# Kernel tuning notes

Measured on AMD Instinct MI355X. Metric: run time of the kernel, lower is better.

## Reference

```python
import jax, jax.numpy as jnp
import numpy as np

DIM = 2048
HIDDEN = 2048
HEADS = 4
HD = HIDDEN // HEADS  # head_dim = 512
EPS = 1e-6
BATCH = 4
SEQ = 2048


def setup_inputs() -> dict:
    key = jax.random.key(0)
    k0, k1, k2, k3 = jax.random.split(key, 4)
    s = 0.02  # typical init scale; keeps exp() input gate well-behaved
    x = jax.random.normal(k0, (BATCH, SEQ, DIM), dtype=jnp.float32)
    W_in = (jax.random.normal(k1, (HIDDEN, DIM), dtype=jnp.float32) * s)
    W_gate = (jax.random.normal(k2, (4 * HIDDEN, HIDDEN), dtype=jnp.float32) * s)
    b_gate = jnp.zeros((4 * HIDDEN,), dtype=jnp.float32)
    rms_w = jnp.ones((HD,), dtype=jnp.float32)
    W_out = (jax.random.normal(k3, (DIM, HIDDEN), dtype=jnp.float32) * s)
    return {"x": x, "W_in": W_in, "W_gate": W_gate, "b_gate": b_gate,
            "rms_w": rms_w, "W_out": W_out}


def reference(x, W_in, W_gate, b_gate, rms_w, W_out):
    B, L, _ = x.shape
    # in_proj then gate_proj (the rearrange round-trip in torch is an identity
    # on the flat hidden dim, so gates come straight from x @ W_in.T)
    xp = x @ W_in.T                                    # (B, L, HIDDEN)
    gates = xp @ W_gate.T + b_gate                     # (B, L, 4*HIDDEN)
    # rearrange 'b l (h d) -> b h l d' with h=HEADS, d=4*HD
    gates = gates.reshape(B, L, HEADS, 4 * HD).transpose(0, 2, 1, 3)
    i_g, f_g, o_g, c_t = jnp.split(gates, 4, axis=-1)  # each (B, H, L, HD)
    i_g = jnp.exp(i_g)            # exponential input gate
    f_g = jax.nn.sigmoid(f_g)
    o_g = jax.nn.sigmoid(o_g)
    c_t = jnp.tanh(c_t)

    # time-major for the recurrent scan: (L, B, H, HD)
    tm = lambda a: jnp.moveaxis(a, 2, 0)

    def step(c, g):
        i, f, o, cd = g
        c = f * c + i * cd                                         # cell update
        c_norm = c * jax.lax.rsqrt(jnp.mean(c * c, axis=-1, keepdims=True) + EPS) * rms_w
        h = o * jnp.tanh(c_norm)
        return c, h

    c0 = jnp.zeros((B, HEADS, HD), dtype=x.dtype)
    _, hs = jax.lax.scan(step, c0, (tm(i_g), tm(f_g), tm(o_g), tm(c_t)))
    # (L, B, H, HD) -> (B, L, H*HD)
    h_out = jnp.moveaxis(hs, 0, 1).reshape(B, L, HIDDEN)
    return h_out @ W_out.T                             # (B, L, DIM)
```

## Files before the change

### kernel.cpp

```cpp
#include <hip/hip_runtime.h>
#include <hip/hip_bf16.h>
#include <stdint.h>

#define DIMN    2048
#define HIDDEN  2048
#define NHEADS  4
#define HDIM    512
#define BATCH   4
#define SEQ     2048
#define NTOK    (BATCH*SEQ)
#define G4      (4*HIDDEN)
#define EPSV    1e-6f
#define CHUNK   128
#define NCHUNK  (SEQ/CHUNK)

typedef short short8 __attribute__((ext_vector_type(8)));
typedef float floatx4 __attribute__((ext_vector_type(4)));

union BV8 { uint4 u; __hip_bfloat16 h[8]; unsigned short s[8]; };

__device__ __forceinline__ float fast_sigmoid(float x) {
    return 1.0f / (1.0f + __expf(-x));
}
__device__ __forceinline__ float fast_tanh(float x) {
    return 1.0f - 2.0f / (__expf(2.0f * x) + 1.0f);
}
__device__ __forceinline__ float b2f(unsigned short u) {
    union { unsigned int ui; float f; } v; v.ui = ((unsigned int)u) << 16; return v.f;
}

__device__ __forceinline__ void gld_lds16(const void* gp, void* lp) {
    __builtin_amdgcn_global_load_lds(
        (const __attribute__((address_space(1))) void*)gp,
        (__attribute__((address_space(3))) void*)lp, 16, 0, 0);
}

__global__ __launch_bounds__(256) void cast_f32_bf16(
    const float* __restrict__ in, __hip_bfloat16* __restrict__ out, int n8)
{
    int i = blockIdx.x * 256 + threadIdx.x;
    if (i >= n8) return;
    const float4* p = (const float4*)(in + (size_t)i * 8);
    float4 a = p[0], b = p[1];
    BV8 v;
    v.h[0] = __float2bfloat16(a.x); v.h[1] = __float2bfloat16(a.y);
    v.h[2] = __float2bfloat16(a.z); v.h[3] = __float2bfloat16(a.w);
    v.h[4] = __float2bfloat16(b.x); v.h[5] = __float2bfloat16(b.y);
    v.h[6] = __float2bfloat16(b.z); v.h[7] = __float2bfloat16(b.w);
    *(uint4*)(out + (size_t)i * 8) = v.u;
}

template <int EPILOGUE, int ASRC>
__global__ __launch_bounds__(512, 2) void gemm256(
    const __hip_bfloat16* __restrict__ A,
    const __hip_bfloat16* __restrict__ Bt,
    void* __restrict__ Cout,
    const float* __restrict__ bias,
    int M, int N, int K, int lda)
{
    __shared__ __align__(16) short sA[2][256 * 64];
    __shared__ __align__(16) short sB[2][256 * 64];

    const int tid  = threadIdx.x;
    const int wave = tid >> 6, lane = tid & 63;
    const int wm = wave >> 2, wn = wave & 3;
    const int quad = lane >> 4, lr = lane & 15;
    const int r8  = lane >> 3;
    const int gcs = ((lane & 7) ^ r8) * 8;
    const int rl7 = lr & 7;

    const int gx   = gridDim.x;
    const int nwg  = gx * gridDim.y;
    const int orig = blockIdx.y * gx + blockIdx.x;
    const int wg   = (orig & 7) * (nwg >> 3) + (orig >> 3);
    const int bm = wg / gx, bn = wg % gx;

    const short* Ag = (const short*)A + (size_t)(bm * 256) * lda;
    const short* Bg = (const short*)Bt + (size_t)(bn * 256) * K;

    floatx4 acc[8][4];
#pragma unroll
    for (int i = 0; i < 8; ++i)
#pragma unroll
        for (int j = 0; j < 4; ++j) acc[i][j] = (floatx4)0.0f;

    const int NT = K >> 6;

    auto stageA = [&](int kt, int qm) {
        const int kb = kt << 6;
        size_t acol;
        if (ASRC == 0) acol = (size_t)(kb + gcs);
        else           acol = (size_t)(((kb >> 9) << 11) + (kb & 511) + gcs);
        short* dst = &sA[kt & 1][0];
#pragma unroll
        for (int e = 0; e < 2; ++e) {
            const int base = qm * 128 + e * 64 + wave * 8;
            const int row  = base + r8;
            const int grow = ((row >> 6) & 1) * 128 + qm * 64 + (row & 63);
            gld_lds16(Ag + (size_t)grow * lda + acol, dst + base * 64);
        }
    };
    auto stageB = [&](int kt, int qn) {
        const int kb = kt << 6;
        short* dst = &sB[kt & 1][0];
#pragma unroll
        for (int e = 0; e < 2; ++e) {
            const int base = qn * 128 + e * 64 + wave * 8;
            const int row  = base + r8;
            const int grow = ((row >> 5) & 3) * 64 + qn * 32 + (row & 31);
            gld_lds16(Bg + (size_t)grow * K + kb + gcs, dst + base * 64);
        }
    };

    stageA(0, 0); stageB(0, 0); stageB(0, 1); stageA(0, 1);
    stageA(1, 0); stageB(1, 0); stageB(1, 1);
    asm volatile("s_waitcnt vmcnt(6)" ::: "memory");
    __builtin_amdgcn_s_barrier();

    short8 av[4][2], b0[2][2], b1[2][2];

    for (int t = 0; t < NT; ++t) {
        const short* lA = &sA[t & 1][0];
        const short* lB = &sB[t & 1][0];

#pragma unroll
        for (int kc = 0; kc < 2; ++kc) {
            const int co = (((kc * 4 + quad) ^ rl7) << 3);
#pragma unroll
            for (int m = 0; m < 4; ++m)
                av[m][kc] = *(const short8*)&lA[(wm * 64 + m * 16 + lr) * 64 + co];
#pragma unroll
            for (int j = 0; j < 2; ++j)
                b0[j][kc] = *(const short8*)&lB[(wn * 32 + j * 16 + lr) * 64 + co];
        }
        if (t + 1 < NT) stageA(t + 1, 1);
        __builtin_amdgcn_s_setprio(1);
#pragma unroll
        for (int m = 0; m < 4; ++m)
#pragma unroll
            for (int j = 0; j < 2; ++j)
#pragma unroll
                for (int kc = 0; kc < 2; ++kc)
                    acc[m][j] = __builtin_amdgcn_mfma_f32_16x16x32_bf16(
                        av[m][kc], b0[j][kc], acc[m][j], 0, 0, 0);
        __builtin_amdgcn_s_setprio(0);
        __builtin_amdgcn_s_barrier();

#pragma unroll
        for (int kc = 0; kc < 2; ++kc) {
            const int co = (((kc * 4 + quad) ^ rl7) << 3);
#pragma unroll
            for (int j = 0; j < 2; ++j)
                b1[j][kc] = *(const short8*)&lB[(128 + wn * 32 + j * 16 + lr) * 64 + co];
        }
        if (t + 2 < NT) stageA(t + 2, 0);
        __builtin_amdgcn_s_setprio(1);
#pragma unroll
        for (int m = 0; m < 4; ++m)
#pragma unroll
            for (int j = 0; j < 2; ++j)
#pragma unroll
                for (int kc = 0; kc < 2; ++kc)
                    acc[m][2 + j] = __builtin_amdgcn_mfma_f32_16x16x32_bf16(
                        av[m][kc], b1[j][kc], acc[m][2 + j], 0, 0, 0);
        __builtin_amdgcn_s_setprio(0);
        __builtin_amdgcn_s_barrier();

#pragma unroll
        for (int kc = 0; kc < 2; ++kc) {
            const int co = (((kc * 4 + quad) ^ rl7) << 3);
#pragma unroll
            for (int m = 0; m < 4; ++m)
                av[m][kc] = *(const short8*)&lA[(128 + wm * 64 + m * 16 + lr) * 64 + co];
        }
        if (t + 2 < NT) stageB(t + 2, 0);
        __builtin_amdgcn_s_setprio(1);
#pragma unroll
        for (int m = 0; m < 4; ++m)
#pragma unroll
            for (int j = 0; j < 2; ++j)
#pragma unroll
                for (int kc = 0; kc < 2; ++kc)
                    acc[4 + m][2 + j] = __builtin_amdgcn_mfma_f32_16x16x32_bf16(
                        av[m][kc], b1[j][kc], acc[4 + m][2 + j], 0, 0, 0);
        __builtin_amdgcn_s_setprio(0);
        __builtin_amdgcn_s_barrier();

        if (t + 2 < NT) stageB(t + 2, 1);
        __builtin_amdgcn_s_setprio(1);
#pragma unroll
        for (int m = 0; m < 4; ++m)
#pragma unroll
            for (int j = 0; j < 2; ++j)
#pragma unroll
                for (int kc = 0; kc < 2; ++kc)
                    acc[4 + m][j] = __builtin_amdgcn_mfma_f32_16x16x32_bf16(
                        av[m][kc], b0[j][kc], acc[4 + m][j], 0, 0, 0);
        __builtin_amdgcn_s_setprio(0);
        if (t < NT - 2)       asm volatile("s_waitcnt vmcnt(6)" ::: "memory");
        else if (t == NT - 2) asm volatile("s_waitcnt vmcnt(0)" ::: "memory");
        __builtin_amdgcn_s_barrier();
    }

    const int colbase = bn * 256 + wn * 64;
    const int rowbase = bm * 256 + wm * 128;

    if (EPILOGUE == 0) {
        __hip_bfloat16* O = (__hip_bfloat16*)Cout;
#pragma unroll
        for (int mt = 0; mt < 8; ++mt)
#pragma unroll
            for (int nt = 0; nt < 4; ++nt)
#pragma unroll
                for (int r = 0; r < 4; ++r) {
                    int row = rowbase + mt * 16 + quad * 4 + r;
                    int col = colbase + nt * 16 + lr;
                    O[(size_t)row * N + col] = __float2bfloat16(acc[mt][nt][r]);
                }
    } else if (EPILOGUE == 1) {
        __hip_bfloat16* O = (__hip_bfloat16*)Cout;
#pragma unroll
        for (int nt = 0; nt < 4; ++nt) {
            int col = colbase + nt * 16 + lr;
            int g = (col >> 9) & 3;
            float bv = bias[col];
#pragma unroll
            for (int mt = 0; mt < 8; ++mt)
#pragma unroll
                for (int r = 0; r < 4; ++r) {
                    int row = rowbase + mt * 16 + quad * 4 + r;
                    float v = acc[mt][nt][r] + bv;
                    if (g == 0)       v = __expf(v);
                    else if (g == 3)  v = fast_tanh(v);
                    else              v = fast_sigmoid(v);
                    O[(size_t)row * N + col] = __float2bfloat16(v);
                }
        }
    } else {
        float* O = (float*)Cout;
#pragma unroll
        for (int mt = 0; mt < 8; ++mt)
#pragma unroll
            for (int nt = 0; nt < 4; ++nt)
#pragma unroll
                for (int r = 0; r < 4; ++r) {
                    int row = rowbase + mt * 16 + quad * 4 + r;
                    int col = colbase + nt * 16 + lr;
                    O[(size_t)row * N + col] = acc[mt][nt][r];
                }
    }
}

struct G16 { unsigned short i[16], f[16], c[16]; };

__device__ __forceinline__ void load_g16(const unsigned short* __restrict__ g,
                                         int t0, G16& o)
{
#pragma unroll
    for (int j = 0; j < 16; ++j) {
        const unsigned short* gp = g + (size_t)(t0 + j) * G4;
        o.i[j] = gp[0]; o.f[j] = gp[512]; o.c[j] = gp[1536];
    }
}
__device__ __forceinline__ void comp_sum16(const G16& gg, float& c, float& P)
{
#pragma unroll
    for (int j = 0; j < 16; ++j) {
        float iv = b2f(gg.i[j]);
        float fv = b2f(gg.f[j]);
        float cd = b2f(gg.c[j]);
        c = fmaf(fv, c, iv * cd);
        P *= fv;
    }
}
__device__ __forceinline__ float comp_store16(const G16& gg, float c,
                                              __hip_bfloat16* __restrict__ cb, int t0)
{
#pragma unroll
    for (int j = 0; j < 16; ++j) {
        float iv = b2f(gg.i[j]);
        float fv = b2f(gg.f[j]);
        float cd = b2f(gg.c[j]);
        c = fmaf(fv, c, iv * cd);
        cb[(size_t)(t0 + j) * HIDDEN] = __float2bfloat16(c);
    }
    return c;
}

__global__ __launch_bounds__(256) void scan_pass1(
    const __hip_bfloat16* __restrict__ gates,
    float* __restrict__ cLast, float* __restrict__ PLast)
{
    int blk = blockIdx.x;
    int dh = blk & 1;
    int j  = (blk >> 1) & 15;
    int bh = blk >> 5;
    int b = bh >> 2, h = bh & 3;
    int d = dh * 256 + threadIdx.x;
    int bhd = bh * 512 + d;

    const unsigned short* g = (const unsigned short*)gates
        + (size_t)(b * SEQ + j * CHUNK) * G4 + h * 2048 + d;

    float c = 0.0f, P = 1.0f;
    G16 A, B;
    load_g16(g, 0, A);
    for (int t0 = 0; t0 < CHUNK; t0 += 32) {
        load_g16(g, t0 + 16, B);
        comp_sum16(A, c, P);
        if (t0 + 32 < CHUNK) load_g16(g, t0 + 32, A);
        comp_sum16(B, c, P);
    }
    cLast[j * 8192 + bhd] = c;
    PLast[j * 8192 + bhd] = P;
}

__global__ __launch_bounds__(256) void scan_pass2(
    const __hip_bfloat16* __restrict__ gates,
    const float* __restrict__ cLast, const float* __restrict__ PLast,
    __hip_bfloat16* __restrict__ cbuf)
{
    int blk = blockIdx.x;
    int dh = blk & 1;
    int j  = (blk >> 1) & 15;
    int bh = blk >> 5;
    int b = bh >> 2, h = bh & 3;
    int d = dh * 256 + threadIdx.x;
    int bhd = bh * 512 + d;

    float c = 0.0f;
    for (int k = 0; k < j; ++k)
        c = fmaf(PLast[k * 8192 + bhd], c, cLast[k * 8192 + bhd]);

    const unsigned short* g = (const unsigned short*)gates
        + (size_t)(b * SEQ + j * CHUNK) * G4 + h * 2048 + d;
    __hip_bfloat16* cb = cbuf
        + (size_t)(b * SEQ + j * CHUNK) * HIDDEN + h * 512 + d;

    G16 A, B;
    load_g16(g, 0, A);
    for (int t0 = 0; t0 < CHUNK; t0 += 32) {
        load_g16(g, t0 + 16, B);
        c = comp_store16(A, c, cb, t0);
        if (t0 + 32 < CHUNK) load_g16(g, t0 + 32, A);
        c = comp_store16(B, c, cb, t0 + 16);
    }
}

__global__ __launch_bounds__(64) void norm_kernel(
    const __hip_bfloat16* __restrict__ cbuf, __hip_bfloat16* __restrict__ gates,
    const float* __restrict__ rms_w)
{
    int blk = blockIdx.x;
    int h = blk & 3;
    int t = (blk >> 2) & (SEQ - 1);
    int b = blk >> 13;
    int lane = threadIdx.x;
    size_t tok = (size_t)(b * SEQ + t);

    BV8 cv; cv.u = *(const uint4*)(cbuf + tok * HIDDEN + h * 512 + lane * 8);
    float cf[8]; float s = 0.0f;
#pragma unroll
    for (int j = 0; j < 8; ++j) { cf[j] = b2f(cv.s[j]); s += cf[j] * cf[j]; }
#pragma unroll
    for (int off = 32; off > 0; off >>= 1) s += __shfl_xor(s, off, 64);
    float rs = rsqrtf(s * (1.0f / 512.0f) + EPSV);

    BV8 ov; ov.u = *(const uint4*)(gates + tok * G4 + h * 2048 + 1024 + lane * 8);
    float4 w0 = *(const float4*)&rms_w[lane * 8];
    float4 w1 = *(const float4*)&rms_w[lane * 8 + 4];
    float w[8] = { w0.x, w0.y, w0.z, w0.w, w1.x, w1.y, w1.z, w1.w };

    BV8 hv;
#pragma unroll
    for (int j = 0; j < 8; ++j) {
        float o = b2f(ov.s[j]);
        hv.h[j] = __float2bfloat16(o * fast_tanh(cf[j] * rs * w[j]));
    }
    *(uint4*)(gates + tok * G4 + h * 2048 + lane * 8) = hv.u;
}

extern "C" void kernel_launch(void* const* d_in, const int* in_sizes, int n_in,
                              void* d_out, int out_size, void* d_ws, size_t ws_size,
                              hipStream_t stream)
{
    const float* x      = (const float*)d_in[0];
    const float* W_in   = (const float*)d_in[1];
    const float* W_gate = (const float*)d_in[2];
    const float* b_gate = (const float*)d_in[3];
    const float* rms_w  = (const float*)d_in[4];
    const float* W_out  = (const float*)d_in[5];
    float* out = (float*)d_out;

    char* base = (char*)d_ws;
    __hip_bfloat16* wgb   = (__hip_bfloat16*)base;
    __hip_bfloat16* xpb   = (__hip_bfloat16*)(base + (((size_t)32) << 20));
    __hip_bfloat16* gates = (__hip_bfloat16*)(base + (((size_t)64) << 20));
    __hip_bfloat16* wib  = gates;
    __hip_bfloat16* xb   = (__hip_bfloat16*)(base + (((size_t)72) << 20));
    __hip_bfloat16* wob  = wgb;
    float* cLast = (float*)(base + (((size_t)8) << 20));
    float* PLast = (float*)(base + (((size_t)8) << 20) + (512 << 10));
    __hip_bfloat16* cbuf = xpb;

    cast_f32_bf16<<<(HIDDEN * DIMN) / 8 / 256, 256, 0, stream>>>(W_in, wib, (HIDDEN * DIMN) / 8);
    cast_f32_bf16<<<(NTOK * DIMN) / 8 / 256, 256, 0, stream>>>(x, xb, (NTOK * DIMN) / 8);
    cast_f32_bf16<<<(G4 * HIDDEN) / 8 / 256, 256, 0, stream>>>(W_gate, wgb, (G4 * HIDDEN) / 8);

    {
        dim3 grid(HIDDEN / 256, NTOK / 256);
        gemm256<0, 0><<<grid, 512, 0, stream>>>(xb, wib, xpb, nullptr,
                                                NTOK, HIDDEN, DIMN, DIMN);
    }
    {
        dim3 grid(G4 / 256, NTOK / 256);
        gemm256<1, 0><<<grid, 512, 0, stream>>>(xpb, wgb, gates, b_gate,
                                                NTOK, G4, HIDDEN, HIDDEN);
    }
    cast_f32_bf16<<<(DIMN * HIDDEN) / 8 / 256, 256, 0, stream>>>(W_out, wob, (DIMN * HIDDEN) / 8);

    scan_pass1<<<BATCH * NHEADS * NCHUNK * 2, 256, 0, stream>>>(gates, cLast, PLast);
    scan_pass2<<<BATCH * NHEADS * NCHUNK * 2, 256, 0, stream>>>(gates, cLast, PLast, cbuf);

    norm_kernel<<<BATCH * SEQ * NHEADS, 64, 0, stream>>>(cbuf, gates, rms_w);

    {
        dim3 grid(DIMN / 256, NTOK / 256);
        gemm256<2, 1><<<grid, 512, 0, stream>>>(gates, wob, out, nullptr,
                                                NTOK, DIMN, HIDDEN, G4);
    }
}
```

Before: 632.9 us.

## Fuse scan pass2 with RMS norm via shared-memory cell buffer

Merges the second scan pass and the per-token RMS-norm/output-gate kernel into one kernel. Each block now covers a full head (512 threads) for one 128-step chunk and keeps the cell states in a 128 KB shared array instead of writing them to global memory. The norm then reads them back from LDS. This removes a global round trip of the cell buffer and one launch. In exchange it cuts the pass-2 grid from 512 to 256 blocks, and the large shared allocation limits occupancy to about one block per CU.

```diff
diff --git a/kernel.cpp b/kernel.cpp
--- a/kernel.cpp
+++ b/kernel.cpp
@@ -273,8 +273,9 @@
         P *= fv;
     }
 }
-__device__ __forceinline__ float comp_store16(const G16& gg, float c,
-                                              __hip_bfloat16* __restrict__ cb, int t0)
+__device__ __forceinline__ float comp_lds16(const G16& gg, float c,
+                                            __hip_bfloat16* __restrict__ sc,
+                                            int t0, int d)
 {
 #pragma unroll
     for (int j = 0; j < 16; ++j) {
@@ -282,7 +283,7 @@
         float fv = b2f(gg.f[j]);
         float cd = b2f(gg.c[j]);
         c = fmaf(fv, c, iv * cd);
-        cb[(size_t)(t0 + j) * HIDDEN] = __float2bfloat16(c);
+        sc[(t0 + j) * HDIM + d] = __float2bfloat16(c);
     }
     return c;
 }
@@ -315,69 +316,65 @@
     PLast[j * 8192 + bhd] = P;
 }
 
-__global__ __launch_bounds__(256) void scan_pass2(
-    const __hip_bfloat16* __restrict__ gates,
+__global__ __launch_bounds__(512) void scan_pass2_norm(
+    const __hip_bfloat16* __restrict__ gates_c,
     const float* __restrict__ cLast, const float* __restrict__ PLast,
-    __hip_bfloat16* __restrict__ cbuf)
-{
+    __hip_bfloat16* __restrict__ gates,
+    const float* __restrict__ rms_w)
+{
+    __shared__ __hip_bfloat16 sc[CHUNK * HDIM];
+
     int blk = blockIdx.x;
-    int dh = blk & 1;
-    int j  = (blk >> 1) & 15;
-    int bh = blk >> 5;
+    int j  = blk & 15;
+    int bh = blk >> 4;
     int b = bh >> 2, h = bh & 3;
-    int d = dh * 256 + threadIdx.x;
+    int d = threadIdx.x;
     int bhd = bh * 512 + d;
 
     float c = 0.0f;
     for (int k = 0; k < j; ++k)
         c = fmaf(PLast[k * 8192 + bhd], c, cLast[k * 8192 + bhd]);
 
-    const unsigned short* g = (const unsigned short*)gates
+    const unsigned short* g = (const unsigned short*)gates_c
         + (size_t)(b * SEQ + j * CHUNK) * G4 + h * 2048 + d;
-    __hip_bfloat16* cb = cbuf
-        + (size_t)(b * SEQ + j * CHUNK) * HIDDEN + h * 512 + d;
 
     G16 A, B;
     load_g16(g, 0, A);
     for (int t0 = 0; t0 < CHUNK; t0 += 32) {
         load_g16(g, t0 + 16, B);
-        c = comp_store16(A, c, cb, t0);
+        c = comp_lds16(A, c, sc, t0, d);
         if (t0 + 32 < CHUNK) load_g16(g, t0 + 32, A);
-        c = comp_store16(B, c, cb, t0 + 16);
-    }
-}
-
-__global__ __launch_bounds__(64) void norm_kernel(
-    const __hip_bfloat16* __restrict__ cbuf, __hip_bfloat16* __restrict__ gates,
-    const float* __restrict__ rms_w)
-{
-    int blk = blockIdx.x;
-    int h = blk & 3;
-    int t = (blk >> 2) & (SEQ - 1);
-    int b = blk >> 13;
-    int lane = threadIdx.x;
-    size_t tok = (size_t)(b * SEQ + t);
-
-    BV8 cv; cv.u = *(const uint4*)(cbuf + tok * HIDDEN + h * 512 + lane * 8);
-    float cf[8]; float s = 0.0f;
-#pragma unroll
-    for (int j = 0; j < 8; ++j) { cf[j] = b2f(cv.s[j]); s += cf[j] * cf[j]; }
-#pragma unroll
-    for (int off = 32; off > 0; off >>= 1) s += __shfl_xor(s, off, 64);
-    float rs = rsqrtf(s * (1.0f / 512.0f) + EPSV);
-
-    BV8 ov; ov.u = *(const uint4*)(gates + tok * G4 + h * 2048 + 1024 + lane * 8);
+        c = comp_lds16(B, c, sc, t0 + 16, d);
+    }
+    __syncthreads();
+
+    const int wave = threadIdx.x >> 6, lane = threadIdx.x & 63;
+
     float4 w0 = *(const float4*)&rms_w[lane * 8];
     float4 w1 = *(const float4*)&rms_w[lane * 8 + 4];
     float w[8] = { w0.x, w0.y, w0.z, w0.w, w1.x, w1.y, w1.z, w1.w };
 
-    BV8 hv;
-#pragma unroll
-    for (int j = 0; j < 8; ++j) {
-        float o = b2f(ov.s[j]);
-        hv.h[j] = __float2bfloat16(o * fast_tanh(cf[j] * rs * w[j]));
-    }
-    *(uint4*)(gates + tok * G4 + h * 2048 + lane * 8) = hv.u;
+    for (int it = 0; it < 16; ++it) {
+        int t = wave * 16 + it;
+        size_t tok = (size_t)(b * SEQ + j * CHUNK + t);
+
+        BV8 cv; cv.u = *(const uint4*)&sc[t * HDIM + lane * 8];
+        float cf[8]; float s = 0.0f;
+#pragma unroll
+        for (int q = 0; q < 8; ++q) { cf[q] = b2f(cv.s[q]); s += cf[q] * cf[q]; }
+#pragma unroll
+        for (int off = 32; off > 0; off >>= 1) s += __shfl_xor(s, off, 64);
+        float rs = rsqrtf(s * (1.0f / 512.0f) + EPSV);
+
+        BV8 ov; ov.u = *(const uint4*)(gates + tok * G4 + h * 2048 + 1024 + lane * 8);
+        BV8 hv;
+#pragma unroll
+        for (int q = 0; q < 8; ++q) {
+            float o = b2f(ov.s[q]);
+            hv.h[q] = __float2bfloat16(o * fast_tanh(cf[q] * rs * w[q]));
+        }
+        *(uint4*)(gates + tok * G4 + h * 2048 + lane * 8) = hv.u;
+    }
 }
 
 extern "C" void kernel_launch(void* const* d_in, const int* in_sizes, int n_in,
@@ -401,7 +398,6 @@
     __hip_bfloat16* wob  = wgb;
     float* cLast = (float*)(base + (((size_t)8) << 20));
     float* PLast = (float*)(base + (((size_t)8) << 20) + (512 << 10));
-    __hip_bfloat16* cbuf = xpb;
 
     cast_f32_bf16<<<(HIDDEN * DIMN) / 8 / 256, 256, 0, stream>>>(W_in, wib, (HIDDEN * DIMN) / 8);
     cast_f32_bf16<<<(NTOK * DIMN) / 8 / 256, 256, 0, stream>>>(x, xb, (NTOK * DIMN) / 8);
@@ -420,9 +416,8 @@
     cast_f32_bf16<<<(DIMN * HIDDEN) / 8 / 256, 256, 0, stream>>>(W_out, wob, (DIMN * HIDDEN) / 8);
 
     scan_pass1<<<BATCH * NHEADS * NCHUNK * 2, 256, 0, stream>>>(gates, cLast, PLast);
-    scan_pass2<<<BATCH * NHEADS * NCHUNK * 2, 256, 0, stream>>>(gates, cLast, PLast, cbuf);
-
-    norm_kernel<<<BATCH * SEQ * NHEADS, 64, 0, stream>>>(cbuf, gates, rms_w);
+    scan_pass2_norm<<<BATCH * NHEADS * NCHUNK, 512, 0, stream>>>(gates, cLast, PLast,
+                                                                 gates, rms_w);
 
     {
         dim3 grid(DIMN / 256, NTOK / 256);
```

Measured after the change: 636.7 us. About the same (+0.6%).
